# Performance work log

Measured on AMD Instinct MI355X. Metric: run time of the kernel, lower is better.

The kernel has to match this reference:

```python
import jax, jax.numpy as jnp
import numpy as np

N = 50000        # num nodes
E = 800000       # num edges (before self-loops)
IN = 256         # in_channels
HID = 32         # hidden_channels per head
HEADS = 8
OUT = 64         # out_channels (layer 2, heads=1)
NEG_SLOPE = 0.2  # PyG GATConv default leaky_relu slope


def setup_inputs() -> dict:
    key = jax.random.key(0)
    ks = jax.random.split(key, 12)
    def rn(k, shape, scale=0.1):
        return jax.random.normal(k, shape, dtype=jnp.float32) * scale
    x = jax.random.normal(ks[0], (N, IN), dtype=jnp.float32)
    edge_index = jax.random.randint(ks[1], (2, E), 0, N, dtype=jnp.int64)
    return {
        "x": x,
        "edge_index": edge_index,
        # GATConv 1: in=256 -> 32 per head, 8 heads, concat
        "W1": rn(ks[2], (IN, HEADS * HID)),
        "att_src1": rn(ks[3], (HEADS, HID)),
        "att_dst1": rn(ks[4], (HEADS, HID)),
        "b1": jnp.zeros((HEADS * HID,), jnp.float32),
        # GATConv 2: in=256 -> 64, 1 head
        "W2": rn(ks[5], (HEADS * HID, OUT)),
        "att_src2": rn(ks[6], (1, OUT)),
        "att_dst2": rn(ks[7], (1, OUT)),
        "b2": jnp.zeros((OUT,), jnp.float32),
    }


def _gat_conv(x, src, dst, W, att_src, att_dst, bias, heads, out_ch):
    """PyG-style GATConv (add_self_loops already applied to src/dst).
    x: [N, F_in]; src/dst: [E']; returns [N, heads*out_ch] (concat)."""
    n = x.shape[0]
    h = (x @ W).reshape(n, heads, out_ch)                     # [N,H,F]
    a_src = jnp.einsum('nhf,hf->nh', h, att_src)              # [N,H]
    a_dst = jnp.einsum('nhf,hf->nh', h, att_dst)
    e = jax.nn.leaky_relu(a_src[src] + a_dst[dst], NEG_SLOPE)  # [E',H]
    # scatter-softmax over incoming edges of each dst node
    m = jax.ops.segment_max(e, dst, num_segments=n)            # [N,H]
    ex = jnp.exp(e - m[dst])
    denom = jax.ops.segment_sum(ex, dst, num_segments=n)       # [N,H]
    alpha = ex / denom[dst]                                    # [E',H]
    msg = alpha[:, :, None] * h[src]                           # [E',H,F]
    out = jax.ops.segment_sum(msg, dst, num_segments=n)        # [N,H,F]
    return out.reshape(n, heads * out_ch) + bias


def reference(x, edge_index, W1, att_src1, att_dst1, b1, W2, att_src2, att_dst2, b2):
    n = x.shape[0]
    loop = jnp.arange(n, dtype=edge_index.dtype)
    src = jnp.concatenate([edge_index[0], loop])  # add self-loops (PyG default)
    dst = jnp.concatenate([edge_index[1], loop])
    h = _gat_conv(x, src, dst, W1, att_src1, att_dst1, b1, HEADS, HID)
    h = jax.nn.relu(h)
    out = _gat_conv(h, src, dst, W2, att_src2, att_dst2, b2, 1, OUT)
    return out
```

## Files before the change

### kernel.cpp

```cpp
#include <hip/hip_runtime.h>
#include <hip/hip_bf16.h>


#define HEADS 8
#define HID 32
#define F1 256
#define F2 64
#define NEG_SLOPE 0.2f
#define CAP 128

typedef __attribute__((ext_vector_type(8))) short bf16x8;
typedef __attribute__((ext_vector_type(4))) float f32x4;
typedef __attribute__((ext_vector_type(8))) unsigned short u16x8;
typedef __attribute__((ext_vector_type(4))) int i32x4;

__device__ __forceinline__ unsigned short f2b(float f) {
    union { float f; unsigned int i; } x; x.f = f;
    unsigned int r = x.i + 0x7fffu + ((x.i >> 16) & 1u);
    return (unsigned short)(r >> 16);
}
__device__ __forceinline__ float b2f(unsigned short u) {
    union { unsigned int i; float f; } x; x.i = ((unsigned int)u) << 16;
    return x.f;
}
__device__ __forceinline__ float leaky(float v) {
    return v > 0.f ? v : NEG_SLOPE * v;
}

__global__ void setup_kernel(const float* __restrict__ W1,
                             const float* __restrict__ W2,
                             unsigned short* __restrict__ W1T,
                             unsigned short* __restrict__ W2T,
                             int* __restrict__ cursor,
                             unsigned short* __restrict__ h1hm,
                             unsigned short* __restrict__ h2b,
                             float* __restrict__ a_src1,
                             float* __restrict__ a_src2, int Nn) {
    const int i = blockIdx.x * 256 + threadIdx.x;
    const int Ns = Nn + 1;
    const int T1 = F1 * F1;
    const int T2 = T1 + F1 * F2;
    const int T3 = T2 + Nn;
    const int T4 = T3 + HEADS * HID;
    const int T5 = T4 + F2;
    const int T6 = T5 + HEADS;
    const int T7 = T6 + 1;
    if (i < T1) {
        const int k = i >> 8, n = i & (F1 - 1);
        W1T[(size_t)n * F1 + k] = f2b(W1[i]);
    } else if (i < T2) {
        const int j = i - T1;
        const int k = j >> 6, n = j & (F2 - 1);
        W2T[(size_t)n * F1 + k] = f2b(W2[j]);
    } else if (i < T3) {
        cursor[i - T2] = 0;
    } else if (i < T4) {
        const int j = i - T3;
        const int h = j >> 5, f = j & 31;
        h1hm[((size_t)h * Ns + Nn) * HID + f] = 0;
    } else if (i < T5) {
        h2b[(size_t)Nn * F2 + (i - T4)] = 0;
    } else if (i < T6) {
        a_src1[(size_t)(i - T5) * Ns + Nn] = -1e30f;
    } else if (i < T7) {
        a_src2[Nn] = -1e30f;
    }
}

__global__ void scatter_kernel(const int* __restrict__ ei, int E,
                               int* __restrict__ cursor,
                               int* __restrict__ bucket) {
    const int e = blockIdx.x * blockDim.x + threadIdx.x;
    if (e >= E) return;
    const int d = ei[E + e];
    const int pos = atomicAdd(&cursor[d], 1);
    if (pos < CAP) __builtin_nontemporal_store(ei[e], &bucket[(size_t)d * CAP + pos]);
}

__global__ void pad_kernel(const int* __restrict__ cursor,
                           int* __restrict__ bucket, int Nn) {
    const int d = blockIdx.x * 256 + threadIdx.x;
    if (d >= Nn) return;
    const int c0 = min(cursor[d], CAP);
    const int ce = min((c0 + 7) & ~7, CAP);
    for (int i = c0; i < ce; ++i)
        __builtin_nontemporal_store(Nn, &bucket[(size_t)d * CAP + i]);
}

template<int BN, bool A_FP32, int OUT_MODE>
__global__ __launch_bounds__(256) void mfma_gemm(
        const void* __restrict__ A,
        const unsigned short* __restrict__ BT,
        void* __restrict__ C, int M, int N, int K, int Mstr) {
    constexpr int BM = 128, BK = 32;
    __shared__ unsigned short As[BM * BK];
    __shared__ unsigned short Bs[BN * BK];
    const int tid = threadIdx.x;
    const int wave = tid >> 6, lane = tid & 63;
    const int quad = lane >> 4, l16 = lane & 15;
    const int brow = blockIdx.x * BM;
    const int bcol = blockIdx.y * BN;

    constexpr int MI = (BN == 128) ? 4 : 2;
    constexpr int NJ = 4;
    const int wm = (BN == 128) ? (wave & 1) * 64 : wave * 32;
    const int wn = (BN == 128) ? (wave >> 1) * 64 : 0;

    f32x4 acc[MI][NJ] = {};

    for (int k0 = 0; k0 < K; k0 += BK) {
#pragma unroll
        for (int it = 0; it < (BM * BK) / (256 * 8); ++it) {
            const int idx = it * 256 + tid;
            const int r = idx >> 2;
            const int kk = (idx & 3) * 8;
            const int gr = brow + r;
            if (A_FP32) {
                const float* Af = (const float*)A;
                float4 a0 = make_float4(0.f, 0.f, 0.f, 0.f);
                float4 a1 = make_float4(0.f, 0.f, 0.f, 0.f);
                if (gr < M) {
                    a0 = *(const float4*)&Af[(size_t)gr * K + k0 + kk];
                    a1 = *(const float4*)&Af[(size_t)gr * K + k0 + kk + 4];
                }
                ushort4 lo, hi;
                lo.x = f2b(a0.x); lo.y = f2b(a0.y); lo.z = f2b(a0.z); lo.w = f2b(a0.w);
                hi.x = f2b(a1.x); hi.y = f2b(a1.y); hi.z = f2b(a1.z); hi.w = f2b(a1.w);
                *(ushort4*)&As[r * BK + kk] = lo;
                *(ushort4*)&As[r * BK + kk + 4] = hi;
            } else {
                const unsigned short* Ab = (const unsigned short*)A;
                uint4 v = make_uint4(0u, 0u, 0u, 0u);
                if (gr < M) v = *(const uint4*)&Ab[(size_t)gr * K + k0 + kk];
                *(uint4*)&As[r * BK + kk] = v;
            }
        }
#pragma unroll
        for (int it = 0; it < (BN * BK) / (256 * 8); ++it) {
            const int idx = it * 256 + tid;
            const int r = idx >> 2;
            const int kk = (idx & 3) * 8;
            const uint4 v = *(const uint4*)&BT[(size_t)(bcol + r) * K + k0 + kk];
            *(uint4*)&Bs[r * BK + kk] = v;
        }
        __syncthreads();
        bf16x8 af[MI], bfr[NJ];
#pragma unroll
        for (int i = 0; i < MI; ++i)
            af[i] = *(const bf16x8*)&As[(wm + i * 16 + l16) * BK + quad * 8];
#pragma unroll
        for (int j = 0; j < NJ; ++j)
            bfr[j] = *(const bf16x8*)&Bs[(wn + j * 16 + l16) * BK + quad * 8];
#pragma unroll
        for (int i = 0; i < MI; ++i)
#pragma unroll
            for (int j = 0; j < NJ; ++j)
                acc[i][j] = __builtin_amdgcn_mfma_f32_16x16x32_bf16(
                    af[i], bfr[j], acc[i][j], 0, 0, 0);
        __syncthreads();
    }
#pragma unroll
    for (int i = 0; i < MI; ++i) {
#pragma unroll
        for (int r = 0; r < 4; ++r) {
            const int row = brow + wm + i * 16 + quad * 4 + r;
            if (row >= M) continue;
#pragma unroll
            for (int j = 0; j < NJ; ++j) {
                const int col = bcol + wn + j * 16 + l16;
                const float v = acc[i][j][r];
                if (OUT_MODE == 1) {
                    ((unsigned short*)C)[(size_t)row * N + col] = f2b(v);
                } else {
                    ((unsigned short*)C)[((size_t)(col >> 5) * Mstr + row) * HID
                                         + (col & 31)] = f2b(v);
                }
            }
        }
    }
}

__global__ void att1_kernel(const unsigned short* __restrict__ h1hm,
                            const float* __restrict__ att_src,
                            const float* __restrict__ att_dst,
                            float* __restrict__ a_src,
                            float* __restrict__ a_dst, int Nn) {
    const int n = blockIdx.x * blockDim.x + threadIdx.x;
    const int h = blockIdx.y;
    if (n >= Nn) return;
    const int Ns = Nn + 1;
    const unsigned short* hp = h1hm + ((size_t)h * Ns + n) * HID;
    const float* as = att_src + h * HID;
    const float* ad = att_dst + h * HID;
    float s = 0.f, dd = 0.f;
#pragma unroll
    for (int f = 0; f < HID; ++f) {
        const float v = b2f(hp[f]);
        s += v * as[f];
        dd += v * ad[f];
    }
    a_src[(size_t)h * Ns + n] = s;
    a_dst[(size_t)h * Ns + n] = dd;
}

__global__ void att2_kernel(const unsigned short* __restrict__ h2b,
                            const float* __restrict__ att_src,
                            const float* __restrict__ att_dst,
                            float* __restrict__ a_src,
                            float* __restrict__ a_dst, int Nn) {
    const int n = blockIdx.x * blockDim.x + threadIdx.x;
    if (n >= Nn) return;
    const unsigned short* hp = h2b + (size_t)n * F2;
    float s = 0.f, d = 0.f;
#pragma unroll
    for (int f = 0; f < F2; ++f) {
        const float v = b2f(hp[f]);
        s += v * att_src[f];
        d += v * att_dst[f];
    }
    a_src[n] = s;
    a_dst[n] = d;
}

__global__ __launch_bounds__(256, 4) void gather1_kernel(
        const int* __restrict__ cursor, const int* __restrict__ bucket,
        const float* __restrict__ a_src, const float* __restrict__ a_dst,
        const unsigned short* __restrict__ h1hm, const float* __restrict__ b1,
        unsigned short* __restrict__ out1b, int Nn) {
    const int h = blockIdx.x & 7;
    const int lane = threadIdx.x & 63;
    const int wv   = threadIdx.x >> 6;
    const int slot = lane >> 2;
    const int cl   = lane & 3;
    const int d = (blockIdx.x >> 3) * 64 + wv * 16 + slot;
    if (d >= Nn) return;
    const int Ns = Nn + 1;

    const unsigned short* hh = h1hm + (size_t)h * Ns * HID;
    const float* asrc = a_src + (size_t)h * Ns;
    const float adst = a_dst[(size_t)h * Ns + d];

    float denom, acc[8];
    {
        const float w = __expf(leaky(asrc[d] + adst));
        const u16x8 v = *(const u16x8*)&hh[(size_t)d * HID + cl * 8];
        denom = w;
#pragma unroll
        for (int q = 0; q < 8; ++q) acc[q] = w * b2f(v[q]);
    }
    const int base = d * CAP;
    const int cnt = min(cursor[d], CAP);
    const int cntp = (cnt + 7) & ~7;
    for (int i = 0; i < cntp; i += 8) {
        const i32x4 sa = __builtin_nontemporal_load((const i32x4*)&bucket[base + i]);
        const i32x4 sb = __builtin_nontemporal_load((const i32x4*)&bucket[base + i + 4]);
        int s[8] = { sa.x, sa.y, sa.z, sa.w, sb.x, sb.y, sb.z, sb.w };
        float e[8];
#pragma unroll
        for (int j = 0; j < 8; ++j) e[j] = asrc[s[j]];
        u16x8 vv[8];
#pragma unroll
        for (int j = 0; j < 8; ++j)
            vv[j] = *(const u16x8*)&hh[(size_t)s[j] * HID + cl * 8];
#pragma unroll
        for (int j = 0; j < 8; ++j) {
            const float w = __expf(leaky(e[j] + adst));
            denom += w;
#pragma unroll
            for (int q = 0; q < 8; ++q) acc[q] += w * b2f(vv[j][q]);
        }
    }
    const float inv = 1.f / denom;
    const int c = h * HID + cl * 8;
    const float4 bv0 = *(const float4*)&b1[c];
    const float4 bv1 = *(const float4*)&b1[c + 4];
    u16x8 o;
    o[0] = f2b(fmaxf(acc[0] * inv + bv0.x, 0.f));
    o[1] = f2b(fmaxf(acc[1] * inv + bv0.y, 0.f));
    o[2] = f2b(fmaxf(acc[2] * inv + bv0.z, 0.f));
    o[3] = f2b(fmaxf(acc[3] * inv + bv0.w, 0.f));
    o[4] = f2b(fmaxf(acc[4] * inv + bv1.x, 0.f));
    o[5] = f2b(fmaxf(acc[5] * inv + bv1.y, 0.f));
    o[6] = f2b(fmaxf(acc[6] * inv + bv1.z, 0.f));
    o[7] = f2b(fmaxf(acc[7] * inv + bv1.w, 0.f));
    __builtin_nontemporal_store(o, (u16x8*)&out1b[(size_t)d * F1 + c]);
}

__global__ __launch_bounds__(256, 4) void gather2_kernel(
        const int* __restrict__ cursor, const int* __restrict__ bucket,
        const float* __restrict__ a_src, const float* __restrict__ a_dst,
        const unsigned short* __restrict__ h2b, const float* __restrict__ b2,
        float* __restrict__ out, int Nn) {
    const int lane = threadIdx.x & 63;
    const int slot = lane >> 4;
    const int l    = lane & 15;
    const int d = blockIdx.x * 16 + (threadIdx.x >> 6) * 4 + slot;
    if (d >= Nn) return;
    const int c = l * 4;

    const float adst = a_dst[d];
    float a0, a1, a2, a3, denom;
    {
        const float w = __expf(leaky(a_src[d] + adst));
        const ushort4 v = *(const ushort4*)&h2b[(size_t)d * F2 + c];
        denom = w;
        a0 = w * b2f(v.x); a1 = w * b2f(v.y);
        a2 = w * b2f(v.z); a3 = w * b2f(v.w);
    }
    const int base = d * CAP;
    const int cnt = min(cursor[d], CAP);
    const int cntp = (cnt + 7) & ~7;
    for (int i = 0; i < cntp; i += 8) {
        const i32x4 sa = __builtin_nontemporal_load((const i32x4*)&bucket[base + i]);
        const i32x4 sb = __builtin_nontemporal_load((const i32x4*)&bucket[base + i + 4]);
        int s[8] = { sa.x, sa.y, sa.z, sa.w, sb.x, sb.y, sb.z, sb.w };
        float e[8];
        ushort4 vv[8];
#pragma unroll
        for (int jj = 0; jj < 8; ++jj) {
            e[jj] = a_src[s[jj]];
            vv[jj] = *(const ushort4*)&h2b[(size_t)s[jj] * F2 + c];
        }
#pragma unroll
        for (int jj = 0; jj < 8; ++jj) {
            const float w = __expf(leaky(e[jj] + adst));
            denom += w;
            a0 += w * b2f(vv[jj].x); a1 += w * b2f(vv[jj].y);
            a2 += w * b2f(vv[jj].z); a3 += w * b2f(vv[jj].w);
        }
    }
    const float inv = 1.f / denom;
    f32x4 o;
    o.x = a0 * inv + b2[c + 0];
    o.y = a1 * inv + b2[c + 1];
    o.z = a2 * inv + b2[c + 2];
    o.w = a3 * inv + b2[c + 3];
    __builtin_nontemporal_store(o, (f32x4*)&out[(size_t)d * F2 + c]);
}

extern "C" void kernel_launch(void* const* d_in, const int* in_sizes, int n_in,
                              void* d_out, int out_size, void* d_ws, size_t ws_size,
                              hipStream_t stream) {
    const float* x        = (const float*)d_in[0];
    const int*   ei       = (const int*)d_in[1];
    const float* W1       = (const float*)d_in[2];
    const float* att_src1 = (const float*)d_in[3];
    const float* att_dst1 = (const float*)d_in[4];
    const float* b1       = (const float*)d_in[5];
    const float* W2       = (const float*)d_in[6];
    const float* att_src2 = (const float*)d_in[7];
    const float* att_dst2 = (const float*)d_in[8];
    const float* b2       = (const float*)d_in[9];
    float* out = (float*)d_out;

    const int Nn = in_sizes[0] / F1;
    const int E  = in_sizes[1] / 2;
    const int Ns = Nn + 1;

    char* p = (char*)d_ws;
    unsigned short* h1hm  = (unsigned short*)p; p += (size_t)Ns * F1 * 2;
    unsigned short* out1b = (unsigned short*)p; p += (size_t)Nn * F1 * 2;
    unsigned short* W1T   = (unsigned short*)p; p += (size_t)F1 * F1 * 2;
    unsigned short* W2T   = (unsigned short*)p; p += (size_t)F2 * F1 * 2;
    unsigned short* h2b   = (unsigned short*)p; p += (size_t)Ns * F2 * 2;
    float* a_src1 = (float*)p; p += (size_t)HEADS * Ns * 4;
    float* a_dst1 = (float*)p; p += (size_t)HEADS * Ns * 4;
    float* a_src2 = (float*)p; p += (size_t)(Nn + 4) * 4;
    float* a_dst2 = (float*)p; p += (size_t)Nn * 4;
    int* cursor  = (int*)p; p += (size_t)Nn * 4;
    int* bucket  = (int*)p; p += (size_t)Nn * CAP * 4;

    {
        const int total = F1 * F1 + F1 * F2 + Nn + HEADS * HID + F2 + HEADS + 1;
        setup_kernel<<<(total + 255) / 256, 256, 0, stream>>>(
            W1, W2, W1T, W2T, cursor, h1hm, h2b, a_src1, a_src2, Nn);
    }
    scatter_kernel<<<(E + 255) / 256, 256, 0, stream>>>(ei, E, cursor, bucket);
    pad_kernel<<<(Nn + 255) / 256, 256, 0, stream>>>(cursor, bucket, Nn);

    {
        dim3 grid((Nn + 127) / 128, F1 / 128);
        mfma_gemm<128, true, 2><<<grid, 256, 0, stream>>>(
            x, W1T, h1hm, Nn, F1, F1, Ns);
    }
    {
        dim3 grid((Nn + 255) / 256, HEADS);
        att1_kernel<<<grid, 256, 0, stream>>>(
            h1hm, att_src1, att_dst1, a_src1, a_dst1, Nn);
    }
    gather1_kernel<<<((Nn + 63) / 64) * 8, 256, 0, stream>>>(
        cursor, bucket, a_src1, a_dst1, h1hm, b1, out1b, Nn);

    {
        dim3 grid((Nn + 127) / 128, F2 / 64);
        mfma_gemm<64, false, 1><<<grid, 256, 0, stream>>>(
            out1b, W2T, h2b, Nn, F2, F1, 0);
    }
    att2_kernel<<<(Nn + 255) / 256, 256, 0, stream>>>(
        h2b, att_src2, att_dst2, a_src2, a_dst2, Nn);
    gather2_kernel<<<(Nn + 15) / 16, 256, 0, stream>>>(
        cursor, bucket, a_src2, a_dst2, h2b, b2, out, Nn);
}
```

Measured before the change: 335.8 us.

## Split each node's edge list across lanes in gather kernels and shrink bucket to 16-bit

The gather kernels now spread each destination node's incoming edges across 8 lane groups, each handling one edge per iteration, and combine the partial sums with xor-shuffle reductions. Before, one lane group walked all of a node's edges serially. The aim is better load balance and more memory-level parallelism for the skewed degree distribution. Bucket entries are stored as unsigned short to halve index traffic. Node ids up to 50000 fit in 16 bits, but larger graphs would silently overflow.

Result: faster. 318.6 us (-5.1%).

```diff
diff --git a/kernel.cpp b/kernel.cpp
--- a/kernel.cpp
+++ b/kernel.cpp
@@ -12,7 +12,6 @@
 typedef __attribute__((ext_vector_type(8))) short bf16x8;
 typedef __attribute__((ext_vector_type(4))) float f32x4;
 typedef __attribute__((ext_vector_type(8))) unsigned short u16x8;
-typedef __attribute__((ext_vector_type(4))) int i32x4;
 
 __device__ __forceinline__ unsigned short f2b(float f) {
     union { float f; unsigned int i; } x; x.f = f;
@@ -69,22 +68,22 @@
 
 __global__ void scatter_kernel(const int* __restrict__ ei, int E,
                                int* __restrict__ cursor,
-                               int* __restrict__ bucket) {
+                               unsigned short* __restrict__ bucket) {
     const int e = blockIdx.x * blockDim.x + threadIdx.x;
     if (e >= E) return;
     const int d = ei[E + e];
     const int pos = atomicAdd(&cursor[d], 1);
-    if (pos < CAP) __builtin_nontemporal_store(ei[e], &bucket[(size_t)d * CAP + pos]);
+    if (pos < CAP) bucket[(size_t)d * CAP + pos] = (unsigned short)ei[e];
 }
 
 __global__ void pad_kernel(const int* __restrict__ cursor,
-                           int* __restrict__ bucket, int Nn) {
+                           unsigned short* __restrict__ bucket, int Nn) {
     const int d = blockIdx.x * 256 + threadIdx.x;
     if (d >= Nn) return;
     const int c0 = min(cursor[d], CAP);
     const int ce = min((c0 + 7) & ~7, CAP);
     for (int i = c0; i < ce; ++i)
-        __builtin_nontemporal_store(Nn, &bucket[(size_t)d * CAP + i]);
+        bucket[(size_t)d * CAP + i] = (unsigned short)Nn;
 }
 
 template<int BN, bool A_FP32, int OUT_MODE>
@@ -222,26 +221,28 @@
     a_dst[n] = d;
 }
 
-__global__ __launch_bounds__(256, 4) void gather1_kernel(
-        const int* __restrict__ cursor, const int* __restrict__ bucket,
+__global__ __launch_bounds__(256, 8) void gather1_kernel(
+        const int* __restrict__ cursor, const unsigned short* __restrict__ bucket,
         const float* __restrict__ a_src, const float* __restrict__ a_dst,
         const unsigned short* __restrict__ h1hm, const float* __restrict__ b1,
         unsigned short* __restrict__ out1b, int Nn) {
     const int h = blockIdx.x & 7;
     const int lane = threadIdx.x & 63;
     const int wv   = threadIdx.x >> 6;
-    const int slot = lane >> 2;
+    const int nd   = lane >> 5;
+    const int slot = (lane >> 2) & 7;
     const int cl   = lane & 3;
-    const int d = (blockIdx.x >> 3) * 64 + wv * 16 + slot;
-    if (d >= Nn) return;
+    int d = (blockIdx.x >> 3) * 8 + wv * 2 + nd;
+    const bool dvalid = d < Nn;
+    if (!dvalid) d = Nn - 1;
     const int Ns = Nn + 1;
 
     const unsigned short* hh = h1hm + (size_t)h * Ns * HID;
     const float* asrc = a_src + (size_t)h * Ns;
     const float adst = a_dst[(size_t)h * Ns + d];
 
-    float denom, acc[8];
-    {
+    float denom = 0.f, acc[8] = {};
+    if (slot == 0) {
         const float w = __expf(leaky(asrc[d] + adst));
         const u16x8 v = *(const u16x8*)&hh[(size_t)d * HID + cl * 8];
         denom = w;
@@ -252,90 +253,91 @@
     const int cnt = min(cursor[d], CAP);
     const int cntp = (cnt + 7) & ~7;
     for (int i = 0; i < cntp; i += 8) {
-        const i32x4 sa = __builtin_nontemporal_load((const i32x4*)&bucket[base + i]);
-        const i32x4 sb = __builtin_nontemporal_load((const i32x4*)&bucket[base + i + 4]);
-        int s[8] = { sa.x, sa.y, sa.z, sa.w, sb.x, sb.y, sb.z, sb.w };
-        float e[8];
-#pragma unroll
-        for (int j = 0; j < 8; ++j) e[j] = asrc[s[j]];
-        u16x8 vv[8];
-#pragma unroll
-        for (int j = 0; j < 8; ++j)
-            vv[j] = *(const u16x8*)&hh[(size_t)s[j] * HID + cl * 8];
-#pragma unroll
-        for (int j = 0; j < 8; ++j) {
-            const float w = __expf(leaky(e[j] + adst));
-            denom += w;
-#pragma unroll
-            for (int q = 0; q < 8; ++q) acc[q] += w * b2f(vv[j][q]);
-        }
-    }
-    const float inv = 1.f / denom;
-    const int c = h * HID + cl * 8;
-    const float4 bv0 = *(const float4*)&b1[c];
-    const float4 bv1 = *(const float4*)&b1[c + 4];
-    u16x8 o;
-    o[0] = f2b(fmaxf(acc[0] * inv + bv0.x, 0.f));
-    o[1] = f2b(fmaxf(acc[1] * inv + bv0.y, 0.f));
-    o[2] = f2b(fmaxf(acc[2] * inv + bv0.z, 0.f));
-    o[3] = f2b(fmaxf(acc[3] * inv + bv0.w, 0.f));
-    o[4] = f2b(fmaxf(acc[4] * inv + bv1.x, 0.f));
-    o[5] = f2b(fmaxf(acc[5] * inv + bv1.y, 0.f));
-    o[6] = f2b(fmaxf(acc[6] * inv + bv1.z, 0.f));
-    o[7] = f2b(fmaxf(acc[7] * inv + bv1.w, 0.f));
-    __builtin_nontemporal_store(o, (u16x8*)&out1b[(size_t)d * F1 + c]);
-}
-
-__global__ __launch_bounds__(256, 4) void gather2_kernel(
-        const int* __restrict__ cursor, const int* __restrict__ bucket,
+        const int sv = bucket[base + i + slot];
+        const float w = __expf(leaky(asrc[sv] + adst));
+        const u16x8 v = *(const u16x8*)&hh[(size_t)sv * HID + cl * 8];
+        denom += w;
+#pragma unroll
+        for (int q = 0; q < 8; ++q) acc[q] += w * b2f(v[q]);
+    }
+#pragma unroll
+    for (int m = 4; m <= 16; m <<= 1) {
+        denom += __shfl_xor(denom, m, 64);
+#pragma unroll
+        for (int q = 0; q < 8; ++q) acc[q] += __shfl_xor(acc[q], m, 64);
+    }
+    if (slot == 0 && dvalid) {
+        const float inv = 1.f / denom;
+        const int c = h * HID + cl * 8;
+        const float4 bv0 = *(const float4*)&b1[c];
+        const float4 bv1 = *(const float4*)&b1[c + 4];
+        u16x8 o;
+        o[0] = f2b(fmaxf(acc[0] * inv + bv0.x, 0.f));
+        o[1] = f2b(fmaxf(acc[1] * inv + bv0.y, 0.f));
+        o[2] = f2b(fmaxf(acc[2] * inv + bv0.z, 0.f));
+        o[3] = f2b(fmaxf(acc[3] * inv + bv0.w, 0.f));
+        o[4] = f2b(fmaxf(acc[4] * inv + bv1.x, 0.f));
+        o[5] = f2b(fmaxf(acc[5] * inv + bv1.y, 0.f));
+        o[6] = f2b(fmaxf(acc[6] * inv + bv1.z, 0.f));
+        o[7] = f2b(fmaxf(acc[7] * inv + bv1.w, 0.f));
+        *(u16x8*)&out1b[(size_t)d * F1 + c] = o;
+    }
+}
+
+__global__ __launch_bounds__(256, 8) void gather2_kernel(
+        const int* __restrict__ cursor, const unsigned short* __restrict__ bucket,
         const float* __restrict__ a_src, const float* __restrict__ a_dst,
         const unsigned short* __restrict__ h2b, const float* __restrict__ b2,
         float* __restrict__ out, int Nn) {
     const int lane = threadIdx.x & 63;
-    const int slot = lane >> 4;
-    const int l    = lane & 15;
-    const int d = blockIdx.x * 16 + (threadIdx.x >> 6) * 4 + slot;
-    if (d >= Nn) return;
-    const int c = l * 4;
+    const int wv   = threadIdx.x >> 6;
+    const int slot = lane >> 3;
+    const int cl   = lane & 7;
+    int d = blockIdx.x * 4 + wv;
+    const bool dvalid = d < Nn;
+    if (!dvalid) d = Nn - 1;
 
     const float adst = a_dst[d];
-    float a0, a1, a2, a3, denom;
-    {
+    float denom = 0.f, acc[8] = {};
+    if (slot == 0) {
         const float w = __expf(leaky(a_src[d] + adst));
-        const ushort4 v = *(const ushort4*)&h2b[(size_t)d * F2 + c];
+        const u16x8 v = *(const u16x8*)&h2b[(size_t)d * F2 + cl * 8];
         denom = w;
-        a0 = w * b2f(v.x); a1 = w * b2f(v.y);
-        a2 = w * b2f(v.z); a3 = w * b2f(v.w);
+#pragma unroll
+        for (int q = 0; q < 8; ++q) acc[q] = w * b2f(v[q]);
     }
     const int base = d * CAP;
     const int cnt = min(cursor[d], CAP);
     const int cntp = (cnt + 7) & ~7;
     for (int i = 0; i < cntp; i += 8) {
-        const i32x4 sa = __builtin_nontemporal_load((const i32x4*)&bucket[base + i]);
-        const i32x4 sb = __builtin_nontemporal_load((const i32x4*)&bucket[base + i + 4]);
-        int s[8] = { sa.x, sa.y, sa.z, sa.w, sb.x, sb.y, sb.z, sb.w };
-        float e[8];
-        ushort4 vv[8];
-#pragma unroll
-        for (int jj = 0; jj < 8; ++jj) {
-            e[jj] = a_src[s[jj]];
-            vv[jj] = *(const ushort4*)&h2b[(size_t)s[jj] * F2 + c];
-        }
-#pragma unroll
-        for (int jj = 0; jj < 8; ++jj) {
-            const float w = __expf(leaky(e[jj] + adst));
-            denom += w;
-            a0 += w * b2f(vv[jj].x); a1 += w * b2f(vv[jj].y);
-            a2 += w * b2f(vv[jj].z); a3 += w * b2f(vv[jj].w);
-        }
-    }
-    const float inv = 1.f / denom;
-    f32x4 o;
-    o.x = a0 * inv + b2[c + 0];
-    o.y = a1 * inv + b2[c + 1];
-    o.z = a2 * inv + b2[c + 2];
-    o.w = a3 * inv + b2[c + 3];
-    __builtin_nontemporal_store(o, (f32x4*)&out[(size_t)d * F2 + c]);
+        const int sv = bucket[base + i + slot];
+        const float w = __expf(leaky(a_src[sv] + adst));
+        const u16x8 v = *(const u16x8*)&h2b[(size_t)sv * F2 + cl * 8];
+        denom += w;
+#pragma unroll
+        for (int q = 0; q < 8; ++q) acc[q] += w * b2f(v[q]);
+    }
+#pragma unroll
+    for (int m = 8; m <= 32; m <<= 1) {
+        denom += __shfl_xor(denom, m, 64);
+#pragma unroll
+        for (int q = 0; q < 8; ++q) acc[q] += __shfl_xor(acc[q], m, 64);
+    }
+    if (slot == 0 && dvalid) {
+        const float inv = 1.f / denom;
+        const int c = cl * 8;
+        f32x4 o0, o1;
+        o0.x = acc[0] * inv + b2[c + 0];
+        o0.y = acc[1] * inv + b2[c + 1];
+        o0.z = acc[2] * inv + b2[c + 2];
+        o0.w = acc[3] * inv + b2[c + 3];
+        o1.x = acc[4] * inv + b2[c + 4];
+        o1.y = acc[5] * inv + b2[c + 5];
+        o1.z = acc[6] * inv + b2[c + 6];
+        o1.w = acc[7] * inv + b2[c + 7];
+        *(f32x4*)&out[(size_t)d * F2 + c] = o0;
+        *(f32x4*)&out[(size_t)d * F2 + c + 4] = o1;
+    }
 }
 
 extern "C" void kernel_launch(void* const* d_in, const int* in_sizes, int n_in,
@@ -368,7 +370,7 @@
     float* a_src2 = (float*)p; p += (size_t)(Nn + 4) * 4;
     float* a_dst2 = (float*)p; p += (size_t)Nn * 4;
     int* cursor  = (int*)p; p += (size_t)Nn * 4;
-    int* bucket  = (int*)p; p += (size_t)Nn * CAP * 4;
+    unsigned short* bucket = (unsigned short*)p; p += (size_t)Nn * CAP * 2;
 
     {
         const int total = F1 * F1 + F1 * F2 + Nn + HEADS * HID + F2 + HEADS + 1;
@@ -388,7 +390,7 @@
         att1_kernel<<<grid, 256, 0, stream>>>(
             h1hm, att_src1, att_dst1, a_src1, a_dst1, Nn);
     }
-    gather1_kernel<<<((Nn + 63) / 64) * 8, 256, 0, stream>>>(
+    gather1_kernel<<<((Nn + 7) / 8) * 8, 256, 0, stream>>>(
         cursor, bucket, a_src1, a_dst1, h1hm, b1, out1b, Nn);
 
     {
@@ -398,6 +400,6 @@
     }
     att2_kernel<<<(Nn + 255) / 256, 256, 0, stream>>>(
         h2b, att_src2, att_dst2, a_src2, a_dst2, Nn);
-    gather2_kernel<<<(Nn + 15) / 16, 256, 0, stream>>>(
+    gather2_kernel<<<(Nn + 3) / 4, 256, 0, stream>>>(
         cursor, bucket, a_src2, a_dst2, h2b, b2, out, Nn);
 }
```

## Sort destination nodes by degree and compress bucket indices to 16-bit

Applied to the files above, without the earlier changes.

Builds a degree histogram, prefix scan and placement pass to produce an order of destination nodes grouped by in-degree. Both gather kernels then process nodes in that order, reducing intra-wave loop-length divergence. Bucket source indices are stored as 16-bit values to halve index traffic, the inner loop is unrolled by 4 instead of 8, and occupancy hints are raised. This adds three small kernels, scatters output writes, and assumes node ids fit in 16 bits.

Result: slower. 591.4 us (+76.1%).

```diff
diff --git a/kernel.cpp b/kernel.cpp
--- a/kernel.cpp
+++ b/kernel.cpp
@@ -12,7 +12,6 @@
 typedef __attribute__((ext_vector_type(8))) short bf16x8;
 typedef __attribute__((ext_vector_type(4))) float f32x4;
 typedef __attribute__((ext_vector_type(8))) unsigned short u16x8;
-typedef __attribute__((ext_vector_type(4))) int i32x4;
 
 __device__ __forceinline__ unsigned short f2b(float f) {
     union { float f; unsigned int i; } x; x.f = f;
@@ -35,7 +34,8 @@
                              unsigned short* __restrict__ h1hm,
                              unsigned short* __restrict__ h2b,
                              float* __restrict__ a_src1,
-                             float* __restrict__ a_src2, int Nn) {
+                             float* __restrict__ a_src2,
+                             int* __restrict__ hist, int Nn) {
     const int i = blockIdx.x * 256 + threadIdx.x;
     const int Ns = Nn + 1;
     const int T1 = F1 * F1;
@@ -45,6 +45,7 @@
     const int T5 = T4 + F2;
     const int T6 = T5 + HEADS;
     const int T7 = T6 + 1;
+    const int T8 = T7 + CAP + 2;
     if (i < T1) {
         const int k = i >> 8, n = i & (F1 - 1);
         W1T[(size_t)n * F1 + k] = f2b(W1[i]);
@@ -64,27 +65,55 @@
         a_src1[(size_t)(i - T5) * Ns + Nn] = -1e30f;
     } else if (i < T7) {
         a_src2[Nn] = -1e30f;
+    } else if (i < T8) {
+        hist[i - T7] = 0;
     }
 }
 
 __global__ void scatter_kernel(const int* __restrict__ ei, int E,
                                int* __restrict__ cursor,
-                               int* __restrict__ bucket) {
+                               unsigned short* __restrict__ bucket) {
     const int e = blockIdx.x * blockDim.x + threadIdx.x;
     if (e >= E) return;
     const int d = ei[E + e];
     const int pos = atomicAdd(&cursor[d], 1);
-    if (pos < CAP) __builtin_nontemporal_store(ei[e], &bucket[(size_t)d * CAP + pos]);
+    if (pos < CAP) bucket[(size_t)d * CAP + pos] = (unsigned short)ei[e];
 }
 
 __global__ void pad_kernel(const int* __restrict__ cursor,
-                           int* __restrict__ bucket, int Nn) {
+                           unsigned short* __restrict__ bucket, int Nn) {
     const int d = blockIdx.x * 256 + threadIdx.x;
     if (d >= Nn) return;
     const int c0 = min(cursor[d], CAP);
-    const int ce = min((c0 + 7) & ~7, CAP);
+    const int ce = min((c0 + 3) & ~3, CAP);
     for (int i = c0; i < ce; ++i)
-        __builtin_nontemporal_store(Nn, &bucket[(size_t)d * CAP + i]);
+        bucket[(size_t)d * CAP + i] = (unsigned short)Nn;
+}
+
+__global__ void hist_kernel(const int* __restrict__ cursor,
+                            int* __restrict__ hist, int Nn) {
+    const int d = blockIdx.x * 256 + threadIdx.x;
+    if (d >= Nn) return;
+    atomicAdd(&hist[min(cursor[d], CAP)], 1);
+}
+
+__global__ void scan_kernel(const int* __restrict__ hist,
+                            int* __restrict__ offsets) {
+    const int t = threadIdx.x;
+    if (t > CAP) return;
+    int s = 0;
+    for (int i = 0; i < t; ++i) s += hist[i];
+    offsets[t] = s;
+}
+
+__global__ void place_kernel(const int* __restrict__ cursor,
+                             int* __restrict__ offsets,
+                             int* __restrict__ order, int Nn) {
+    const int d = blockIdx.x * 256 + threadIdx.x;
+    if (d >= Nn) return;
+    const int c = min(cursor[d], CAP);
+    const int pos = atomicAdd(&offsets[c], 1);
+    order[pos] = d;
 }
 
 template<int BN, bool A_FP32, int OUT_MODE>
@@ -222,8 +251,9 @@
     a_dst[n] = d;
 }
 
-__global__ __launch_bounds__(256, 4) void gather1_kernel(
-        const int* __restrict__ cursor, const int* __restrict__ bucket,
+__global__ __launch_bounds__(256, 8) void gather1_kernel(
+        const int* __restrict__ cursor, const unsigned short* __restrict__ bucket,
+        const int* __restrict__ order,
         const float* __restrict__ a_src, const float* __restrict__ a_dst,
         const unsigned short* __restrict__ h1hm, const float* __restrict__ b1,
         unsigned short* __restrict__ out1b, int Nn) {
@@ -232,8 +262,9 @@
     const int wv   = threadIdx.x >> 6;
     const int slot = lane >> 2;
     const int cl   = lane & 3;
-    const int d = (blockIdx.x >> 3) * 64 + wv * 16 + slot;
-    if (d >= Nn) return;
+    const int gi = (blockIdx.x >> 3) * 64 + wv * 16 + slot;
+    if (gi >= Nn) return;
+    const int d = order[gi];
     const int Ns = Nn + 1;
 
     const unsigned short* hh = h1hm + (size_t)h * Ns * HID;
@@ -250,25 +281,25 @@
     }
     const int base = d * CAP;
     const int cnt = min(cursor[d], CAP);
-    const int cntp = (cnt + 7) & ~7;
-    for (int i = 0; i < cntp; i += 8) {
-        const i32x4 sa = __builtin_nontemporal_load((const i32x4*)&bucket[base + i]);
-        const i32x4 sb = __builtin_nontemporal_load((const i32x4*)&bucket[base + i + 4]);
-        int s[8] = { sa.x, sa.y, sa.z, sa.w, sb.x, sb.y, sb.z, sb.w };
-        float e[8];
-#pragma unroll
-        for (int j = 0; j < 8; ++j) e[j] = asrc[s[j]];
-        u16x8 vv[8];
-#pragma unroll
-        for (int j = 0; j < 8; ++j)
-            vv[j] = *(const u16x8*)&hh[(size_t)s[j] * HID + cl * 8];
-#pragma unroll
-        for (int j = 0; j < 8; ++j) {
-            const float w = __expf(leaky(e[j] + adst));
-            denom += w;
-#pragma unroll
-            for (int q = 0; q < 8; ++q) acc[q] += w * b2f(vv[j][q]);
-        }
+    const int cntp = (cnt + 3) & ~3;
+    for (int i = 0; i < cntp; i += 4) {
+        const ushort4 s4 = *(const ushort4*)&bucket[base + i];
+        const int s0 = s4.x, s1 = s4.y, s2 = s4.z, s3 = s4.w;
+        const float e0 = asrc[s0], e1 = asrc[s1];
+        const float e2 = asrc[s2], e3 = asrc[s3];
+        const u16x8 v0 = *(const u16x8*)&hh[(size_t)s0 * HID + cl * 8];
+        const u16x8 v1 = *(const u16x8*)&hh[(size_t)s1 * HID + cl * 8];
+        const u16x8 v2 = *(const u16x8*)&hh[(size_t)s2 * HID + cl * 8];
+        const u16x8 v3 = *(const u16x8*)&hh[(size_t)s3 * HID + cl * 8];
+        const float w0 = __expf(leaky(e0 + adst));
+        const float w1 = __expf(leaky(e1 + adst));
+        const float w2 = __expf(leaky(e2 + adst));
+        const float w3 = __expf(leaky(e3 + adst));
+        denom += w0 + w1 + w2 + w3;
+#pragma unroll
+        for (int q = 0; q < 8; ++q)
+            acc[q] += w0 * b2f(v0[q]) + w1 * b2f(v1[q])
+                    + w2 * b2f(v2[q]) + w3 * b2f(v3[q]);
     }
     const float inv = 1.f / denom;
     const int c = h * HID + cl * 8;
@@ -283,19 +314,21 @@
     o[5] = f2b(fmaxf(acc[5] * inv + bv1.y, 0.f));
     o[6] = f2b(fmaxf(acc[6] * inv + bv1.z, 0.f));
     o[7] = f2b(fmaxf(acc[7] * inv + bv1.w, 0.f));
-    __builtin_nontemporal_store(o, (u16x8*)&out1b[(size_t)d * F1 + c]);
-}
-
-__global__ __launch_bounds__(256, 4) void gather2_kernel(
-        const int* __restrict__ cursor, const int* __restrict__ bucket,
+    *(u16x8*)&out1b[(size_t)d * F1 + c] = o;
+}
+
+__global__ __launch_bounds__(256, 8) void gather2_kernel(
+        const int* __restrict__ cursor, const unsigned short* __restrict__ bucket,
+        const int* __restrict__ order,
         const float* __restrict__ a_src, const float* __restrict__ a_dst,
         const unsigned short* __restrict__ h2b, const float* __restrict__ b2,
         float* __restrict__ out, int Nn) {
     const int lane = threadIdx.x & 63;
     const int slot = lane >> 4;
     const int l    = lane & 15;
-    const int d = blockIdx.x * 16 + (threadIdx.x >> 6) * 4 + slot;
-    if (d >= Nn) return;
+    const int gi = blockIdx.x * 16 + (threadIdx.x >> 6) * 4 + slot;
+    if (gi >= Nn) return;
+    const int d = order[gi];
     const int c = l * 4;
 
     const float adst = a_dst[d];
@@ -309,25 +342,25 @@
     }
     const int base = d * CAP;
     const int cnt = min(cursor[d], CAP);
-    const int cntp = (cnt + 7) & ~7;
-    for (int i = 0; i < cntp; i += 8) {
-        const i32x4 sa = __builtin_nontemporal_load((const i32x4*)&bucket[base + i]);
-        const i32x4 sb = __builtin_nontemporal_load((const i32x4*)&bucket[base + i + 4]);
-        int s[8] = { sa.x, sa.y, sa.z, sa.w, sb.x, sb.y, sb.z, sb.w };
-        float e[8];
-        ushort4 vv[8];
-#pragma unroll
-        for (int jj = 0; jj < 8; ++jj) {
-            e[jj] = a_src[s[jj]];
-            vv[jj] = *(const ushort4*)&h2b[(size_t)s[jj] * F2 + c];
-        }
-#pragma unroll
-        for (int jj = 0; jj < 8; ++jj) {
-            const float w = __expf(leaky(e[jj] + adst));
-            denom += w;
-            a0 += w * b2f(vv[jj].x); a1 += w * b2f(vv[jj].y);
-            a2 += w * b2f(vv[jj].z); a3 += w * b2f(vv[jj].w);
-        }
+    const int cntp = (cnt + 3) & ~3;
+    for (int i = 0; i < cntp; i += 4) {
+        const ushort4 s4 = *(const ushort4*)&bucket[base + i];
+        const int s0 = s4.x, s1 = s4.y, s2 = s4.z, s3 = s4.w;
+        const float e0 = a_src[s0], e1 = a_src[s1];
+        const float e2 = a_src[s2], e3 = a_src[s3];
+        const ushort4 v0 = *(const ushort4*)&h2b[(size_t)s0 * F2 + c];
+        const ushort4 v1 = *(const ushort4*)&h2b[(size_t)s1 * F2 + c];
+        const ushort4 v2 = *(const ushort4*)&h2b[(size_t)s2 * F2 + c];
+        const ushort4 v3 = *(const ushort4*)&h2b[(size_t)s3 * F2 + c];
+        const float w0 = __expf(leaky(e0 + adst));
+        const float w1 = __expf(leaky(e1 + adst));
+        const float w2 = __expf(leaky(e2 + adst));
+        const float w3 = __expf(leaky(e3 + adst));
+        denom += w0 + w1 + w2 + w3;
+        a0 += w0 * b2f(v0.x) + w1 * b2f(v1.x) + w2 * b2f(v2.x) + w3 * b2f(v3.x);
+        a1 += w0 * b2f(v0.y) + w1 * b2f(v1.y) + w2 * b2f(v2.y) + w3 * b2f(v3.y);
+        a2 += w0 * b2f(v0.z) + w1 * b2f(v1.z) + w2 * b2f(v2.z) + w3 * b2f(v3.z);
+        a3 += w0 * b2f(v0.w) + w1 * b2f(v1.w) + w2 * b2f(v2.w) + w3 * b2f(v3.w);
     }
     const float inv = 1.f / denom;
     f32x4 o;
@@ -335,7 +368,7 @@
     o.y = a1 * inv + b2[c + 1];
     o.z = a2 * inv + b2[c + 2];
     o.w = a3 * inv + b2[c + 3];
-    __builtin_nontemporal_store(o, (f32x4*)&out[(size_t)d * F2 + c]);
+    *(f32x4*)&out[(size_t)d * F2 + c] = o;
 }
 
 extern "C" void kernel_launch(void* const* d_in, const int* in_sizes, int n_in,
@@ -368,15 +401,22 @@
     float* a_src2 = (float*)p; p += (size_t)(Nn + 4) * 4;
     float* a_dst2 = (float*)p; p += (size_t)Nn * 4;
     int* cursor  = (int*)p; p += (size_t)Nn * 4;
-    int* bucket  = (int*)p; p += (size_t)Nn * CAP * 4;
-
-    {
-        const int total = F1 * F1 + F1 * F2 + Nn + HEADS * HID + F2 + HEADS + 1;
+    int* order   = (int*)p; p += (size_t)Nn * 4;
+    int* hist    = (int*)p; p += (size_t)(CAP + 2) * 4;
+    int* offsets = (int*)p; p += (size_t)(CAP + 2) * 4;
+    unsigned short* bucket = (unsigned short*)p; p += (size_t)Nn * CAP * 2;
+
+    {
+        const int total = F1 * F1 + F1 * F2 + Nn + HEADS * HID + F2 + HEADS + 1
+                          + CAP + 2;
         setup_kernel<<<(total + 255) / 256, 256, 0, stream>>>(
-            W1, W2, W1T, W2T, cursor, h1hm, h2b, a_src1, a_src2, Nn);
+            W1, W2, W1T, W2T, cursor, h1hm, h2b, a_src1, a_src2, hist, Nn);
     }
     scatter_kernel<<<(E + 255) / 256, 256, 0, stream>>>(ei, E, cursor, bucket);
     pad_kernel<<<(Nn + 255) / 256, 256, 0, stream>>>(cursor, bucket, Nn);
+    hist_kernel<<<(Nn + 255) / 256, 256, 0, stream>>>(cursor, hist, Nn);
+    scan_kernel<<<1, 256, 0, stream>>>(hist, offsets);
+    place_kernel<<<(Nn + 255) / 256, 256, 0, stream>>>(cursor, offsets, order, Nn);
 
     {
         dim3 grid((Nn + 127) / 128, F1 / 128);
@@ -389,7 +429,7 @@
             h1hm, att_src1, att_dst1, a_src1, a_dst1, Nn);
     }
     gather1_kernel<<<((Nn + 63) / 64) * 8, 256, 0, stream>>>(
-        cursor, bucket, a_src1, a_dst1, h1hm, b1, out1b, Nn);
+        cursor, bucket, order, a_src1, a_dst1, h1hm, b1, out1b, Nn);
 
     {
         dim3 grid((Nn + 127) / 128, F2 / 64);
@@ -399,5 +439,5 @@
     att2_kernel<<<(Nn + 255) / 256, 256, 0, stream>>>(
         h2b, att_src2, att_dst2, a_src2, a_dst2, Nn);
     gather2_kernel<<<(Nn + 15) / 16, 256, 0, stream>>>(
-        cursor, bucket, a_src2, a_dst2, h2b, b2, out, Nn);
-}
+        cursor, bucket, order, a_src2, a_dst2, h2b, b2, out, Nn);
+}
```

## Store edge buckets as 16-bit indices and software-pipeline layer-1 gather

Applied to the files above, without the earlier changes.

Source indices in the per-destination bucket are now stored as unsigned short instead of int, halving the bucket footprint and the index traffic in the scatter, pad and both gather kernels. Padding now always fills at least 8 slots. gather1 is rewritten to process 4 neighbours per step while prefetching the next group's features and indices two steps ahead, and its occupancy hint rises from 4 to 6 blocks per CU. Nontemporal load and store hints are dropped. The 16-bit indices only hold while the node count stays below 65536, and the extra prefetch registers compete with the higher occupancy target.

Result: faster. 300.5 us (-10.5%).

```diff
diff --git a/kernel.cpp b/kernel.cpp
--- a/kernel.cpp
+++ b/kernel.cpp
@@ -12,7 +12,6 @@
 typedef __attribute__((ext_vector_type(8))) short bf16x8;
 typedef __attribute__((ext_vector_type(4))) float f32x4;
 typedef __attribute__((ext_vector_type(8))) unsigned short u16x8;
-typedef __attribute__((ext_vector_type(4))) int i32x4;
 
 __device__ __forceinline__ unsigned short f2b(float f) {
     union { float f; unsigned int i; } x; x.f = f;
@@ -69,22 +68,22 @@
 
 __global__ void scatter_kernel(const int* __restrict__ ei, int E,
                                int* __restrict__ cursor,
-                               int* __restrict__ bucket) {
+                               unsigned short* __restrict__ bucket) {
     const int e = blockIdx.x * blockDim.x + threadIdx.x;
     if (e >= E) return;
     const int d = ei[E + e];
     const int pos = atomicAdd(&cursor[d], 1);
-    if (pos < CAP) __builtin_nontemporal_store(ei[e], &bucket[(size_t)d * CAP + pos]);
+    if (pos < CAP) bucket[(size_t)d * CAP + pos] = (unsigned short)ei[e];
 }
 
 __global__ void pad_kernel(const int* __restrict__ cursor,
-                           int* __restrict__ bucket, int Nn) {
+                           unsigned short* __restrict__ bucket, int Nn) {
     const int d = blockIdx.x * 256 + threadIdx.x;
     if (d >= Nn) return;
     const int c0 = min(cursor[d], CAP);
-    const int ce = min((c0 + 7) & ~7, CAP);
+    const int ce = min(max((c0 + 7) & ~7, 8), CAP);
     for (int i = c0; i < ce; ++i)
-        __builtin_nontemporal_store(Nn, &bucket[(size_t)d * CAP + i]);
+        bucket[(size_t)d * CAP + i] = (unsigned short)Nn;
 }
 
 template<int BN, bool A_FP32, int OUT_MODE>
@@ -222,8 +221,8 @@
     a_dst[n] = d;
 }
 
-__global__ __launch_bounds__(256, 4) void gather1_kernel(
-        const int* __restrict__ cursor, const int* __restrict__ bucket,
+__global__ __launch_bounds__(256, 6) void gather1_kernel(
+        const int* __restrict__ cursor, const unsigned short* __restrict__ bucket,
         const float* __restrict__ a_src, const float* __restrict__ a_dst,
         const unsigned short* __restrict__ h1hm, const float* __restrict__ b1,
         unsigned short* __restrict__ out1b, int Nn) {
@@ -248,27 +247,47 @@
 #pragma unroll
         for (int q = 0; q < 8; ++q) acc[q] = w * b2f(v[q]);
     }
-    const int base = d * CAP;
+    const unsigned short* bk = bucket + (size_t)d * CAP;
     const int cnt = min(cursor[d], CAP);
-    const int cntp = (cnt + 7) & ~7;
-    for (int i = 0; i < cntp; i += 8) {
-        const i32x4 sa = __builtin_nontemporal_load((const i32x4*)&bucket[base + i]);
-        const i32x4 sb = __builtin_nontemporal_load((const i32x4*)&bucket[base + i + 4]);
-        int s[8] = { sa.x, sa.y, sa.z, sa.w, sb.x, sb.y, sb.z, sb.w };
-        float e[8];
-#pragma unroll
-        for (int j = 0; j < 8; ++j) e[j] = asrc[s[j]];
-        u16x8 vv[8];
-#pragma unroll
-        for (int j = 0; j < 8; ++j)
-            vv[j] = *(const u16x8*)&hh[(size_t)s[j] * HID + cl * 8];
-#pragma unroll
-        for (int j = 0; j < 8; ++j) {
-            const float w = __expf(leaky(e[j] + adst));
-            denom += w;
-#pragma unroll
-            for (int q = 0; q < 8; ++q) acc[q] += w * b2f(vv[j][q]);
-        }
+    const int NR = max((cnt + 3) >> 2, 2);
+
+    ushort4 sc = *(const ushort4*)&bk[0];
+    ushort4 sn = *(const ushort4*)&bk[4];
+    float ec[4];
+    u16x8 vc[4];
+    {
+        const int i0 = sc.x, i1 = sc.y, i2 = sc.z, i3 = sc.w;
+        ec[0] = asrc[i0]; ec[1] = asrc[i1]; ec[2] = asrc[i2]; ec[3] = asrc[i3];
+        vc[0] = *(const u16x8*)&hh[(size_t)i0 * HID + cl * 8];
+        vc[1] = *(const u16x8*)&hh[(size_t)i1 * HID + cl * 8];
+        vc[2] = *(const u16x8*)&hh[(size_t)i2 * HID + cl * 8];
+        vc[3] = *(const u16x8*)&hh[(size_t)i3 * HID + cl * 8];
+    }
+    for (int r = 0; r < NR; ++r) {
+        float en[4];
+        u16x8 vn[4];
+        {
+            const int i0 = sn.x, i1 = sn.y, i2 = sn.z, i3 = sn.w;
+            en[0] = asrc[i0]; en[1] = asrc[i1]; en[2] = asrc[i2]; en[3] = asrc[i3];
+            vn[0] = *(const u16x8*)&hh[(size_t)i0 * HID + cl * 8];
+            vn[1] = *(const u16x8*)&hh[(size_t)i1 * HID + cl * 8];
+            vn[2] = *(const u16x8*)&hh[(size_t)i2 * HID + cl * 8];
+            vn[3] = *(const u16x8*)&hh[(size_t)i3 * HID + cl * 8];
+        }
+        const int r2 = min(r + 2, NR - 1);
+        const ushort4 s2 = *(const ushort4*)&bk[r2 * 4];
+        const float w0 = __expf(leaky(ec[0] + adst));
+        const float w1 = __expf(leaky(ec[1] + adst));
+        const float w2 = __expf(leaky(ec[2] + adst));
+        const float w3 = __expf(leaky(ec[3] + adst));
+        denom += w0 + w1 + w2 + w3;
+#pragma unroll
+        for (int q = 0; q < 8; ++q)
+            acc[q] += w0 * b2f(vc[0][q]) + w1 * b2f(vc[1][q])
+                    + w2 * b2f(vc[2][q]) + w3 * b2f(vc[3][q]);
+        sc = sn; sn = s2;
+#pragma unroll
+        for (int j = 0; j < 4; ++j) { ec[j] = en[j]; vc[j] = vn[j]; }
     }
     const float inv = 1.f / denom;
     const int c = h * HID + cl * 8;
@@ -283,11 +302,11 @@
     o[5] = f2b(fmaxf(acc[5] * inv + bv1.y, 0.f));
     o[6] = f2b(fmaxf(acc[6] * inv + bv1.z, 0.f));
     o[7] = f2b(fmaxf(acc[7] * inv + bv1.w, 0.f));
-    __builtin_nontemporal_store(o, (u16x8*)&out1b[(size_t)d * F1 + c]);
+    *(u16x8*)&out1b[(size_t)d * F1 + c] = o;
 }
 
 __global__ __launch_bounds__(256, 4) void gather2_kernel(
-        const int* __restrict__ cursor, const int* __restrict__ bucket,
+        const int* __restrict__ cursor, const unsigned short* __restrict__ bucket,
         const float* __restrict__ a_src, const float* __restrict__ a_dst,
         const unsigned short* __restrict__ h2b, const float* __restrict__ b2,
         float* __restrict__ out, int Nn) {
@@ -307,13 +326,13 @@
         a0 = w * b2f(v.x); a1 = w * b2f(v.y);
         a2 = w * b2f(v.z); a3 = w * b2f(v.w);
     }
-    const int base = d * CAP;
+    const unsigned short* bk = bucket + (size_t)d * CAP;
     const int cnt = min(cursor[d], CAP);
     const int cntp = (cnt + 7) & ~7;
     for (int i = 0; i < cntp; i += 8) {
-        const i32x4 sa = __builtin_nontemporal_load((const i32x4*)&bucket[base + i]);
-        const i32x4 sb = __builtin_nontemporal_load((const i32x4*)&bucket[base + i + 4]);
-        int s[8] = { sa.x, sa.y, sa.z, sa.w, sb.x, sb.y, sb.z, sb.w };
+        const ushort4 sa = *(const ushort4*)&bk[i];
+        const ushort4 sb = *(const ushort4*)&bk[i + 4];
+        const int s[8] = { sa.x, sa.y, sa.z, sa.w, sb.x, sb.y, sb.z, sb.w };
         float e[8];
         ushort4 vv[8];
 #pragma unroll
@@ -335,7 +354,7 @@
     o.y = a1 * inv + b2[c + 1];
     o.z = a2 * inv + b2[c + 2];
     o.w = a3 * inv + b2[c + 3];
-    __builtin_nontemporal_store(o, (f32x4*)&out[(size_t)d * F2 + c]);
+    *(f32x4*)&out[(size_t)d * F2 + c] = o;
 }
 
 extern "C" void kernel_launch(void* const* d_in, const int* in_sizes, int n_in,
@@ -368,7 +387,7 @@
     float* a_src2 = (float*)p; p += (size_t)(Nn + 4) * 4;
     float* a_dst2 = (float*)p; p += (size_t)Nn * 4;
     int* cursor  = (int*)p; p += (size_t)Nn * 4;
-    int* bucket  = (int*)p; p += (size_t)Nn * CAP * 4;
+    unsigned short* bucket = (unsigned short*)p; p += (size_t)Nn * CAP * 2;
 
     {
         const int total = F1 * F1 + F1 * F2 + Nn + HEADS * HID + F2 + HEADS + 1;
```
